# Optimization experiments

Hardware: AMD Instinct MI355X
Metric: run time of the kernel (lower is better)

The kernel has to match this reference:

```python
import jax, jax.numpy as jnp
import numpy as np

B, T, D, U, P, E = 32, 10, 10, 50, 50, 256
EPS_ATTN = 1e-8
EPS_LN = 1e-5


def _layer_norm(x, w, b):
    mu = jnp.mean(x, axis=-1, keepdims=True)
    var = jnp.mean((x - mu) ** 2, axis=-1, keepdims=True)
    return (x - mu) / jnp.sqrt(var + EPS_LN) * w + b


def setup_inputs() -> dict:
    key = jax.random.key(0)
    ks = jax.random.split(key, 8)
    xavier = float(np.sqrt(2.0 / (E + E)))
    return {
        "Q": jax.random.normal(ks[0], (B, T, U, E), dtype=jnp.float32),
        "K": jax.random.normal(ks[1], (B, D, P, E), dtype=jnp.float32),
        "V": jax.random.normal(ks[2], (B, D, P, E), dtype=jnp.float32),
        "attention_mask": jnp.zeros((B, T, D, U, P), dtype=jnp.float32),
        "W1": jax.random.normal(ks[3], (E, E), dtype=jnp.float32) * xavier,
        "b1": jnp.zeros((E,), dtype=jnp.float32),
        "W2": jax.random.normal(ks[4], (E, E), dtype=jnp.float32) * xavier,
        "b2": jnp.zeros((E,), dtype=jnp.float32),
        "ln1_w": jnp.ones((E,), dtype=jnp.float32),
        "ln1_b": jnp.zeros((E,), dtype=jnp.float32),
        "ln2_w": jnp.ones((E,), dtype=jnp.float32),
        "ln2_b": jnp.zeros((E,), dtype=jnp.float32),
    }


def reference(Q, K, V, attention_mask, W1, b1, W2, b2, ln1_w, ln1_b, ln2_w, ln2_b):
    # dk = max(1.0, emb_dim); scale = sqrt(dk) + eps
    scale = jnp.sqrt(jnp.asarray(float(max(1.0, Q.shape[-1])), dtype=Q.dtype)) + EPS_ATTN
    # (B,T,D,U,P) attention logits
    qk = jnp.einsum("btue,bdpe->btdup", Q, K) / scale + attention_mask
    score = jax.nn.softmax(qk, axis=-1)
    v_att = jnp.einsum("btdup,bdpe->btdue", score, V)  # (B,T,D,U,E)
    x = Q[:, :, None, :, :] + v_att  # broadcast over doc dim
    x = _layer_norm(x, ln1_w, ln1_b)
    ffn = jnp.maximum(x @ W1.T + b1, 0.0) @ W2.T + b2
    return _layer_norm(ffn + x, ln2_w, ln2_b)
```

## Files before the change

### kernel.cpp

```cpp
#include <hip/hip_runtime.h>
#include <math.h>

#define Bsz 32
#define Tt  10
#define Dd  10
#define Uu  50
#define Pp  50
#define Ee  256

typedef __attribute__((ext_vector_type(8))) short bf16x8;
typedef __attribute__((ext_vector_type(4))) float f32x4;

#define STH 264
#define STV 72
#define STS 72

#define K1_OFF_V 0
#define K1_OFF_S 36864
#define K1_OFF_R 46080
#define K1_SMEM  47104

#define K2_OFF_H 0
#define K2_OFF_R 33792
#define K2_SMEM  35840

__device__ __forceinline__ unsigned short f2bf(float f) {
    unsigned u = __builtin_bit_cast(unsigned, f);
    u += 0x7fffu + ((u >> 16) & 1u);
    return (unsigned short)(u >> 16);
}
__device__ __forceinline__ float bf2f(unsigned short h) {
    unsigned u = ((unsigned)h) << 16;
    return __builtin_bit_cast(float, u);
}
__device__ __forceinline__ bf16x8 ldfrag(const unsigned short* p, int stride, int r0, int c0, int lane) {
    return *(const bf16x8*)(p + (size_t)(r0 + (lane & 15)) * stride + c0 + ((lane >> 4) << 3));
}
__device__ __forceinline__ bf16x8 gfrag49(const float* __restrict__ base, int n, int k0, int lane) {
    int row = n + (lane & 15);
    row = row > 49 ? 49 : row;
    const int col = k0 + ((lane >> 4) << 3);
    const float4 a = *(const float4*)(base + (size_t)row * 256 + col);
    const float4 b = *(const float4*)(base + (size_t)row * 256 + col + 4);
    bf16x8 r;
    r[0] = (short)f2bf(a.x); r[1] = (short)f2bf(a.y); r[2] = (short)f2bf(a.z); r[3] = (short)f2bf(a.w);
    r[4] = (short)f2bf(b.x); r[5] = (short)f2bf(b.y); r[6] = (short)f2bf(b.z); r[7] = (short)f2bf(b.w);
    return r;
}
__device__ __forceinline__ bf16x8 wfrag(const unsigned short* wbf, const float* wf, int use_ws,
                                        int n, int k0, int lane) {
    const int row = n + (lane & 15);
    const int col = k0 + ((lane >> 4) << 3);
    if (use_ws) {
        return *(const bf16x8*)(wbf + (size_t)row * 256 + col);
    }
    const float4 a = *(const float4*)(wf + (size_t)row * 256 + col);
    const float4 b = *(const float4*)(wf + (size_t)row * 256 + col + 4);
    bf16x8 r;
    r[0] = (short)f2bf(a.x); r[1] = (short)f2bf(a.y); r[2] = (short)f2bf(a.z); r[3] = (short)f2bf(a.w);
    r[4] = (short)f2bf(b.x); r[5] = (short)f2bf(b.y); r[6] = (short)f2bf(b.z); r[7] = (short)f2bf(b.w);
    return r;
}

__global__ void convert_w_kernel(const float* __restrict__ W1, const float* __restrict__ W2,
                                 unsigned short* __restrict__ ws) {
    int i4 = (blockIdx.x * 256 + threadIdx.x) * 4;
    float4 a = *(const float4*)(W1 + i4);
    ushort4 oa; oa.x = f2bf(a.x); oa.y = f2bf(a.y); oa.z = f2bf(a.z); oa.w = f2bf(a.w);
    *(ushort4*)(ws + i4) = oa;
    float4 b = *(const float4*)(W2 + i4);
    ushort4 ob; ob.x = f2bf(b.x); ob.y = f2bf(b.y); ob.z = f2bf(b.z); ob.w = f2bf(b.w);
    *(ushort4*)(ws + 65536 + i4) = ob;
}

__global__ __launch_bounds__(512, 4) void attn_kernel(
    const float* __restrict__ Q,  const float* __restrict__ K,
    const float* __restrict__ V,  const float* __restrict__ Msk,
    const float* __restrict__ ln1w, const float* __restrict__ ln1b,
    float* __restrict__ out)
{
    __shared__ __align__(16) unsigned char smem[K1_SMEM];
    unsigned short* sVt = (unsigned short*)(smem + K1_OFF_V);
    unsigned short* sS  = (unsigned short*)(smem + K1_OFF_S);
    float*          red = (float*)(smem + K1_OFF_R);

    const int tid  = threadIdx.x;
    const int lane = tid & 63;
    const int wave = tid >> 6;
    const int quad = lane >> 4;
    const int l15  = lane & 15;

    const int btd = ((blockIdx.x & 7) * 400) + (blockIdx.x >> 3);
    const int b   = btd / (Tt * Dd);
    const int rem = btd % (Tt * Dd);
    const int t   = rem / Dd;
    const int d   = rem % Dd;

    const float* Qb = Q + ((size_t)(b * Tt + t) * Uu) * Ee;
    const float* Kb = K + ((size_t)(b * Dd + d) * Pp) * Ee;
    const float* Vb = V + ((size_t)(b * Dd + d) * Pp) * Ee;
    const float* Mb = Msk + ((size_t)((b * Tt + t) * Dd + d) * Uu) * Pp;
    float*       Xb = out + ((size_t)btd * Uu) * Ee;

    if (wave < 4) {
        const int mt = wave;
        int arow = mt * 16 + l15; if (arow > 49) arow = 49;
        const float* qrow = Qb + (size_t)arow * Ee + (quad << 3);
        f32x4 acc[4];
        #pragma unroll
        for (int i = 0; i < 4; ++i) acc[i] = (f32x4){0.f, 0.f, 0.f, 0.f};
        #pragma unroll
        for (int k0 = 0; k0 < 256; k0 += 32) {
            float4 qa = *(const float4*)(qrow + k0);
            float4 qb = *(const float4*)(qrow + k0 + 4);
            bf16x8 a;
            a[0] = (short)f2bf(qa.x); a[1] = (short)f2bf(qa.y); a[2] = (short)f2bf(qa.z); a[3] = (short)f2bf(qa.w);
            a[4] = (short)f2bf(qb.x); a[5] = (short)f2bf(qb.y); a[6] = (short)f2bf(qb.z); a[7] = (short)f2bf(qb.w);
            #pragma unroll
            for (int nt = 0; nt < 4; ++nt) {
                bf16x8 bf = gfrag49(Kb, nt << 4, k0, lane);
                acc[nt] = __builtin_amdgcn_mfma_f32_16x16x32_bf16(a, bf, acc[nt], 0, 0, 0);
            }
        }
        float l[4][4];
        #pragma unroll
        for (int nt = 0; nt < 4; ++nt) {
            int p = (nt << 4) + l15;
            #pragma unroll
            for (int r = 0; r < 4; ++r) {
                int u = mt * 16 + (quad << 2) + r;
                float v = acc[nt][r] * 0.0625f;
                if (p < Pp) { if (u < Uu) v += Mb[u * Pp + p]; }
                else v = -1e30f;
                l[nt][r] = v;
            }
        }
        #pragma unroll
        for (int r = 0; r < 4; ++r) {
            float m = fmaxf(fmaxf(l[0][r], l[1][r]), fmaxf(l[2][r], l[3][r]));
            #pragma unroll
            for (int msk = 1; msk < 16; msk <<= 1) m = fmaxf(m, __shfl_xor(m, msk));
            float e0 = __expf(l[0][r] - m), e1 = __expf(l[1][r] - m);
            float e2 = __expf(l[2][r] - m), e3 = __expf(l[3][r] - m);
            float s = e0 + e1 + e2 + e3;
            #pragma unroll
            for (int msk = 1; msk < 16; msk <<= 1) s += __shfl_xor(s, msk);
            float inv = 1.0f / s;
            int u = mt * 16 + (quad << 2) + r;
            sS[u * STS +  0 + l15] = f2bf(e0 * inv);
            sS[u * STS + 16 + l15] = f2bf(e1 * inv);
            sS[u * STS + 32 + l15] = f2bf(e2 * inv);
            sS[u * STS + 48 + l15] = f2bf(e3 * inv);
        }
    } else {
        const int lt = tid - 256;
        #pragma unroll 4
        for (int i = lt; i < 12800; i += 256) {
            int p = i >> 8, e = i & 255;
            sVt[e * STV + p] = f2bf(Vb[p * Ee + e]);
        }
        for (int i = lt; i < 3584; i += 256) {
            int p = 50 + (i >> 8), e = i & 255;
            sVt[e * STV + p] = 0;
        }
    }
    __syncthreads();

    {
        const int mt = wave >> 1;
        const int nh = (wave & 1) << 7;
        f32x4 acc[8];
        #pragma unroll
        for (int i = 0; i < 8; ++i) acc[i] = (f32x4){0.f, 0.f, 0.f, 0.f};
        #pragma unroll
        for (int k0 = 0; k0 < 64; k0 += 32) {
            bf16x8 a = ldfrag(sS, STS, mt << 4, k0, lane);
            #pragma unroll
            for (int nt = 0; nt < 8; ++nt) {
                bf16x8 bf = ldfrag(sVt, STV, nh + (nt << 4), k0, lane);
                acc[nt] = __builtin_amdgcn_mfma_f32_16x16x32_bf16(a, bf, acc[nt], 0, 0, 0);
            }
        }
        float s1[4] = {0.f, 0.f, 0.f, 0.f}, s2[4] = {0.f, 0.f, 0.f, 0.f};
        #pragma unroll
        for (int nt = 0; nt < 8; ++nt) {
            int e = nh + (nt << 4) + l15;
            #pragma unroll
            for (int r = 0; r < 4; ++r) {
                int u = (mt << 4) + (quad << 2) + r;
                float x = 0.f;
                if (u < Uu) x = acc[nt][r] + Qb[(size_t)u * Ee + e];
                acc[nt][r] = x;
                s1[r] += x; s2[r] += x * x;
            }
        }
        #pragma unroll
        for (int msk = 1; msk < 16; msk <<= 1) {
            #pragma unroll
            for (int r = 0; r < 4; ++r) { s1[r] += __shfl_xor(s1[r], msk); s2[r] += __shfl_xor(s2[r], msk); }
        }
        if (l15 == 0) {
            #pragma unroll
            for (int r = 0; r < 4; ++r) {
                int u = (mt << 4) + (quad << 2) + r;
                red[u * 4 + (wave & 1) * 2 + 0] = s1[r];
                red[u * 4 + (wave & 1) * 2 + 1] = s2[r];
            }
        }
        __syncthreads();
        #pragma unroll
        for (int r = 0; r < 4; ++r) {
            int u = (mt << 4) + (quad << 2) + r;
            if (u < Uu) {
                float sum = red[u * 4 + 0] + red[u * 4 + 2];
                float sq  = red[u * 4 + 1] + red[u * 4 + 3];
                float mu = sum * (1.0f / 256.0f);
                float var = sq * (1.0f / 256.0f) - mu * mu;
                float rstd = rsqrtf(var + 1e-5f);
                #pragma unroll
                for (int nt = 0; nt < 8; ++nt) {
                    int e = nh + (nt << 4) + l15;
                    Xb[(size_t)u * Ee + e] = (acc[nt][r] - mu) * rstd * ln1w[e] + ln1b[e];
                }
            }
        }
    }
}

__global__ __launch_bounds__(512, 4) void ffn_kernel(
    const float* __restrict__ W1, const float* __restrict__ b1,
    const float* __restrict__ W2, const float* __restrict__ b2,
    const float* __restrict__ ln2w, const float* __restrict__ ln2b,
    const unsigned short* __restrict__ wsbf, int use_ws,
    float* __restrict__ out)
{
    __shared__ __align__(16) unsigned char smem[K2_SMEM];
    unsigned short* sH   = (unsigned short*)(smem + K2_OFF_H);
    float*          red2 = (float*)(smem + K2_OFF_R);

    const int tid  = threadIdx.x;
    const int lane = tid & 63;
    const int wave = tid >> 6;
    const int quad = lane >> 4;
    const int l15  = lane & 15;

    const int btd = blockIdx.x;
    const float* Xb = out + (size_t)btd * Uu * Ee;
    float*       Ob = out + (size_t)btd * Uu * Ee;

    const int mp = wave >> 2;
    const int nq = wave & 3;

    {
        f32x4 acc2[2][4];
        #pragma unroll
        for (int mi = 0; mi < 2; ++mi)
            #pragma unroll
            for (int nt = 0; nt < 4; ++nt) acc2[mi][nt] = (f32x4){0.f, 0.f, 0.f, 0.f};
        float b1v[4];
        #pragma unroll
        for (int nt = 0; nt < 4; ++nt) b1v[nt] = b1[(nq << 6) + (nt << 4) + l15];
        #pragma unroll
        for (int k0 = 0; k0 < 256; k0 += 32) {
            bf16x8 a0 = gfrag49(Xb, (mp << 5),      k0, lane);
            bf16x8 a1 = gfrag49(Xb, (mp << 5) + 16, k0, lane);
            #pragma unroll
            for (int nt = 0; nt < 4; ++nt) {
                bf16x8 bf = wfrag(wsbf, W1, use_ws, (nq << 6) + (nt << 4), k0, lane);
                acc2[0][nt] = __builtin_amdgcn_mfma_f32_16x16x32_bf16(a0, bf, acc2[0][nt], 0, 0, 0);
                acc2[1][nt] = __builtin_amdgcn_mfma_f32_16x16x32_bf16(a1, bf, acc2[1][nt], 0, 0, 0);
            }
        }
        #pragma unroll
        for (int mi = 0; mi < 2; ++mi)
            #pragma unroll
            for (int nt = 0; nt < 4; ++nt) {
                int j = (nq << 6) + (nt << 4) + l15;
                #pragma unroll
                for (int r = 0; r < 4; ++r) {
                    int u = (mp << 5) + (mi << 4) + (quad << 2) + r;
                    sH[u * STH + j] = f2bf(fmaxf(acc2[mi][nt][r] + b1v[nt], 0.f));
                }
            }
    }
    __syncthreads();

    {
        f32x4 acc2[2][4];
        #pragma unroll
        for (int mi = 0; mi < 2; ++mi)
            #pragma unroll
            for (int nt = 0; nt < 4; ++nt) acc2[mi][nt] = (f32x4){0.f, 0.f, 0.f, 0.f};
        float b2v[4], w2l[4], b2l[4];
        #pragma unroll
        for (int nt = 0; nt < 4; ++nt) {
            int j = (nq << 6) + (nt << 4) + l15;
            b2v[nt] = b2[j]; w2l[nt] = ln2w[j]; b2l[nt] = ln2b[j];
        }
        #pragma unroll
        for (int k0 = 0; k0 < 256; k0 += 32) {
            bf16x8 a0 = ldfrag(sH, STH, (mp << 5),      k0, lane);
            bf16x8 a1 = ldfrag(sH, STH, (mp << 5) + 16, k0, lane);
            #pragma unroll
            for (int nt = 0; nt < 4; ++nt) {
                bf16x8 bf = wfrag(wsbf + 65536, W2, use_ws, (nq << 6) + (nt << 4), k0, lane);
                acc2[0][nt] = __builtin_amdgcn_mfma_f32_16x16x32_bf16(a0, bf, acc2[0][nt], 0, 0, 0);
                acc2[1][nt] = __builtin_amdgcn_mfma_f32_16x16x32_bf16(a1, bf, acc2[1][nt], 0, 0, 0);
            }
        }
        float s1[2][4], s2[2][4];
        #pragma unroll
        for (int mi = 0; mi < 2; ++mi)
            #pragma unroll
            for (int r = 0; r < 4; ++r) { s1[mi][r] = 0.f; s2[mi][r] = 0.f; }
        #pragma unroll
        for (int mi = 0; mi < 2; ++mi)
            #pragma unroll
            for (int nt = 0; nt < 4; ++nt) {
                int j = (nq << 6) + (nt << 4) + l15;
                #pragma unroll
                for (int r = 0; r < 4; ++r) {
                    int u = (mp << 5) + (mi << 4) + (quad << 2) + r;
                    float xr = (u < Uu) ? Xb[(size_t)u * Ee + j] : 0.f;
                    float y = acc2[mi][nt][r] + b2v[nt] + xr;
                    acc2[mi][nt][r] = y;
                    s1[mi][r] += y; s2[mi][r] += y * y;
                }
            }
        #pragma unroll
        for (int msk = 1; msk < 16; msk <<= 1)
            #pragma unroll
            for (int mi = 0; mi < 2; ++mi)
                #pragma unroll
                for (int r = 0; r < 4; ++r) {
                    s1[mi][r] += __shfl_xor(s1[mi][r], msk);
                    s2[mi][r] += __shfl_xor(s2[mi][r], msk);
                }
        if (l15 == 0) {
            #pragma unroll
            for (int mi = 0; mi < 2; ++mi)
                #pragma unroll
                for (int r = 0; r < 4; ++r) {
                    int u = (mp << 5) + (mi << 4) + (quad << 2) + r;
                    red2[u * 8 + nq * 2 + 0] = s1[mi][r];
                    red2[u * 8 + nq * 2 + 1] = s2[mi][r];
                }
        }
        __syncthreads();
        #pragma unroll
        for (int mi = 0; mi < 2; ++mi)
            #pragma unroll
            for (int r = 0; r < 4; ++r) {
                int u = (mp << 5) + (mi << 4) + (quad << 2) + r;
                if (u < Uu) {
                    float sum = red2[u * 8 + 0] + red2[u * 8 + 2] + red2[u * 8 + 4] + red2[u * 8 + 6];
                    float sq  = red2[u * 8 + 1] + red2[u * 8 + 3] + red2[u * 8 + 5] + red2[u * 8 + 7];
                    float mu = sum * (1.0f / 256.0f);
                    float var = sq * (1.0f / 256.0f) - mu * mu;
                    float rstd = rsqrtf(var + 1e-5f);
                    #pragma unroll
                    for (int nt = 0; nt < 4; ++nt) {
                        int j = (nq << 6) + (nt << 4) + l15;
                        Ob[(size_t)u * Ee + j] = (acc2[mi][nt][r] - mu) * rstd * w2l[nt] + b2l[nt];
                    }
                }
            }
    }
}

extern "C" void kernel_launch(void* const* d_in, const int* in_sizes, int n_in,
                              void* d_out, int out_size, void* d_ws, size_t ws_size,
                              hipStream_t stream) {
    const float* Q    = (const float*)d_in[0];
    const float* K    = (const float*)d_in[1];
    const float* V    = (const float*)d_in[2];
    const float* M    = (const float*)d_in[3];
    const float* W1   = (const float*)d_in[4];
    const float* b1   = (const float*)d_in[5];
    const float* W2   = (const float*)d_in[6];
    const float* b2   = (const float*)d_in[7];
    const float* ln1w = (const float*)d_in[8];
    const float* ln1b = (const float*)d_in[9];
    const float* ln2w = (const float*)d_in[10];
    const float* ln2b = (const float*)d_in[11];
    float* out = (float*)d_out;

    int use_ws = (ws_size >= 262144) ? 1 : 0;
    const unsigned short* wsbf = (const unsigned short*)d_ws;
    if (use_ws) {
        convert_w_kernel<<<64, 256, 0, stream>>>(W1, W2, (unsigned short*)d_ws);
    }
    attn_kernel<<<Bsz * Tt * Dd, 512, 0, stream>>>(Q, K, V, M, ln1w, ln1b, out);
    ffn_kernel<<<Bsz * Tt * Dd, 512, 0, stream>>>(W1, b1, W2, b2, ln2w, ln2b,
                                                  wsbf, use_ws, out);
}
```

Measured before the change: 673.9 us.

## Tile FFN over flattened rows in 128-row blocks instead of per-50-row group

The FFN kernel now treats all B*T*D*U rows as one flat matrix and gives each block 128 rows, instead of 50 rows padded to 64. This removes the padding waste of about 22% in the MFMA work and reuses each weight fragment across four M-tiles per wave, which cuts weight traffic per row. In exchange the block uses twice the LDS and needs more accumulator registers, which may lower occupancy. The total row count of 160000 divides evenly by 128, so no bounds checks are needed.

```diff
diff --git a/kernel.cpp b/kernel.cpp
--- a/kernel.cpp
+++ b/kernel.cpp
@@ -21,8 +21,9 @@
 #define K1_SMEM  47104
 
 #define K2_OFF_H 0
-#define K2_OFF_R 33792
-#define K2_SMEM  35840
+#define K2_OFF_R 67584
+#define K2_SMEM  71680
+#define FFN_BM 128
 
 __device__ __forceinline__ unsigned short f2bf(float f) {
     unsigned u = __builtin_bit_cast(unsigned, f);
@@ -47,6 +48,16 @@
     r[4] = (short)f2bf(b.x); r[5] = (short)f2bf(b.y); r[6] = (short)f2bf(b.z); r[7] = (short)f2bf(b.w);
     return r;
 }
+__device__ __forceinline__ bf16x8 xfrag(const float* __restrict__ base, int n, int k0, int lane) {
+    const int row = n + (lane & 15);
+    const int col = k0 + ((lane >> 4) << 3);
+    const float4 a = *(const float4*)(base + (size_t)row * 256 + col);
+    const float4 b = *(const float4*)(base + (size_t)row * 256 + col + 4);
+    bf16x8 r;
+    r[0] = (short)f2bf(a.x); r[1] = (short)f2bf(a.y); r[2] = (short)f2bf(a.z); r[3] = (short)f2bf(a.w);
+    r[4] = (short)f2bf(b.x); r[5] = (short)f2bf(b.y); r[6] = (short)f2bf(b.z); r[7] = (short)f2bf(b.w);
+    return r;
+}
 __device__ __forceinline__ bf16x8 wfrag(const unsigned short* wbf, const float* wf, int use_ws,
                                         int n, int k0, int lane) {
     const int row = n + (lane & 15);
@@ -244,53 +255,55 @@
     const int quad = lane >> 4;
     const int l15  = lane & 15;
 
-    const int btd = blockIdx.x;
-    const float* Xb = out + (size_t)btd * Uu * Ee;
-    float*       Ob = out + (size_t)btd * Uu * Ee;
-
-    const int mp = wave >> 2;
+    const int mw = wave >> 2;
     const int nq = wave & 3;
 
+    const size_t rowbase = (size_t)blockIdx.x * FFN_BM;
+    const float* Xb = out + rowbase * Ee;
+    float*       Ob = out + rowbase * Ee;
+
     {
-        f32x4 acc2[2][4];
-        #pragma unroll
-        for (int mi = 0; mi < 2; ++mi)
-            #pragma unroll
-            for (int nt = 0; nt < 4; ++nt) acc2[mi][nt] = (f32x4){0.f, 0.f, 0.f, 0.f};
+        f32x4 acc[4][4];
+        #pragma unroll
+        for (int mi = 0; mi < 4; ++mi)
+            #pragma unroll
+            for (int nt = 0; nt < 4; ++nt) acc[mi][nt] = (f32x4){0.f, 0.f, 0.f, 0.f};
         float b1v[4];
         #pragma unroll
         for (int nt = 0; nt < 4; ++nt) b1v[nt] = b1[(nq << 6) + (nt << 4) + l15];
         #pragma unroll
         for (int k0 = 0; k0 < 256; k0 += 32) {
-            bf16x8 a0 = gfrag49(Xb, (mp << 5),      k0, lane);
-            bf16x8 a1 = gfrag49(Xb, (mp << 5) + 16, k0, lane);
+            bf16x8 a[4];
+            #pragma unroll
+            for (int mi = 0; mi < 4; ++mi) a[mi] = xfrag(Xb, (mw << 6) + (mi << 4), k0, lane);
             #pragma unroll
             for (int nt = 0; nt < 4; ++nt) {
                 bf16x8 bf = wfrag(wsbf, W1, use_ws, (nq << 6) + (nt << 4), k0, lane);
-                acc2[0][nt] = __builtin_amdgcn_mfma_f32_16x16x32_bf16(a0, bf, acc2[0][nt], 0, 0, 0);
-                acc2[1][nt] = __builtin_amdgcn_mfma_f32_16x16x32_bf16(a1, bf, acc2[1][nt], 0, 0, 0);
-            }
-        }
-        #pragma unroll
-        for (int mi = 0; mi < 2; ++mi)
+                #pragma unroll
+                for (int mi = 0; mi < 4; ++mi)
+                    acc[mi][nt] = __builtin_amdgcn_mfma_f32_16x16x32_bf16(a[mi], bf, acc[mi][nt], 0, 0, 0);
+            }
+        }
+        #pragma unroll
+        for (int mi = 0; mi < 4; ++mi)
             #pragma unroll
             for (int nt = 0; nt < 4; ++nt) {
                 int j = (nq << 6) + (nt << 4) + l15;
                 #pragma unroll
                 for (int r = 0; r < 4; ++r) {
-                    int u = (mp << 5) + (mi << 4) + (quad << 2) + r;
-                    sH[u * STH + j] = f2bf(fmaxf(acc2[mi][nt][r] + b1v[nt], 0.f));
+                    int u = (mw << 6) + (mi << 4) + (quad << 2) + r;
+                    sH[u * STH + j] = f2bf(fmaxf(acc[mi][nt][r] + b1v[nt], 0.f));
                 }
             }
     }
     __syncthreads();
 
     {
-        f32x4 acc2[2][4];
-        #pragma unroll
-        for (int mi = 0; mi < 2; ++mi)
-            #pragma unroll
-            for (int nt = 0; nt < 4; ++nt) acc2[mi][nt] = (f32x4){0.f, 0.f, 0.f, 0.f};
+        f32x4 acc[4][4];
+        #pragma unroll
+        for (int mi = 0; mi < 4; ++mi)
+            #pragma unroll
+            for (int nt = 0; nt < 4; ++nt) acc[mi][nt] = (f32x4){0.f, 0.f, 0.f, 0.f};
         float b2v[4], w2l[4], b2l[4];
         #pragma unroll
         for (int nt = 0; nt < 4; ++nt) {
@@ -299,70 +312,62 @@
         }
         #pragma unroll
         for (int k0 = 0; k0 < 256; k0 += 32) {
-            bf16x8 a0 = ldfrag(sH, STH, (mp << 5),      k0, lane);
-            bf16x8 a1 = ldfrag(sH, STH, (mp << 5) + 16, k0, lane);
+            bf16x8 a[4];
+            #pragma unroll
+            for (int mi = 0; mi < 4; ++mi) a[mi] = ldfrag(sH, STH, (mw << 6) + (mi << 4), k0, lane);
             #pragma unroll
             for (int nt = 0; nt < 4; ++nt) {
                 bf16x8 bf = wfrag(wsbf + 65536, W2, use_ws, (nq << 6) + (nt << 4), k0, lane);
-                acc2[0][nt] = __builtin_amdgcn_mfma_f32_16x16x32_bf16(a0, bf, acc2[0][nt], 0, 0, 0);
-                acc2[1][nt] = __builtin_amdgcn_mfma_f32_16x16x32_bf16(a1, bf, acc2[1][nt], 0, 0, 0);
-            }
-        }
-        float s1[2][4], s2[2][4];
-        #pragma unroll
-        for (int mi = 0; mi < 2; ++mi)
-            #pragma unroll
-            for (int r = 0; r < 4; ++r) { s1[mi][r] = 0.f; s2[mi][r] = 0.f; }
-        #pragma unroll
-        for (int mi = 0; mi < 2; ++mi)
+                #pragma unroll
+                for (int mi = 0; mi < 4; ++mi)
+                    acc[mi][nt] = __builtin_amdgcn_mfma_f32_16x16x32_bf16(a[mi], bf, acc[mi][nt], 0, 0, 0);
+            }
+        }
+        #pragma unroll
+        for (int mi = 0; mi < 4; ++mi) {
+            float s1[4] = {0.f, 0.f, 0.f, 0.f}, s2[4] = {0.f, 0.f, 0.f, 0.f};
             #pragma unroll
             for (int nt = 0; nt < 4; ++nt) {
                 int j = (nq << 6) + (nt << 4) + l15;
                 #pragma unroll
                 for (int r = 0; r < 4; ++r) {
-                    int u = (mp << 5) + (mi << 4) + (quad << 2) + r;
-                    float xr = (u < Uu) ? Xb[(size_t)u * Ee + j] : 0.f;
-                    float y = acc2[mi][nt][r] + b2v[nt] + xr;
-                    acc2[mi][nt][r] = y;
-                    s1[mi][r] += y; s2[mi][r] += y * y;
-                }
-            }
-        #pragma unroll
-        for (int msk = 1; msk < 16; msk <<= 1)
-            #pragma unroll
-            for (int mi = 0; mi < 2; ++mi)
+                    int u = (mw << 6) + (mi << 4) + (quad << 2) + r;
+                    float y = acc[mi][nt][r] + b2v[nt] + Xb[(size_t)u * Ee + j];
+                    acc[mi][nt][r] = y;
+                    s1[r] += y; s2[r] += y * y;
+                }
+            }
+            #pragma unroll
+            for (int msk = 1; msk < 16; msk <<= 1)
                 #pragma unroll
                 for (int r = 0; r < 4; ++r) {
-                    s1[mi][r] += __shfl_xor(s1[mi][r], msk);
-                    s2[mi][r] += __shfl_xor(s2[mi][r], msk);
-                }
-        if (l15 == 0) {
-            #pragma unroll
-            for (int mi = 0; mi < 2; ++mi)
+                    s1[r] += __shfl_xor(s1[r], msk);
+                    s2[r] += __shfl_xor(s2[r], msk);
+                }
+            if (l15 == 0) {
                 #pragma unroll
                 for (int r = 0; r < 4; ++r) {
-                    int u = (mp << 5) + (mi << 4) + (quad << 2) + r;
-                    red2[u * 8 + nq * 2 + 0] = s1[mi][r];
-                    red2[u * 8 + nq * 2 + 1] = s2[mi][r];
-                }
+                    int u = (mw << 6) + (mi << 4) + (quad << 2) + r;
+                    red2[u * 8 + nq * 2 + 0] = s1[r];
+                    red2[u * 8 + nq * 2 + 1] = s2[r];
+                }
+            }
         }
         __syncthreads();
         #pragma unroll
-        for (int mi = 0; mi < 2; ++mi)
+        for (int mi = 0; mi < 4; ++mi)
             #pragma unroll
             for (int r = 0; r < 4; ++r) {
-                int u = (mp << 5) + (mi << 4) + (quad << 2) + r;
-                if (u < Uu) {
-                    float sum = red2[u * 8 + 0] + red2[u * 8 + 2] + red2[u * 8 + 4] + red2[u * 8 + 6];
-                    float sq  = red2[u * 8 + 1] + red2[u * 8 + 3] + red2[u * 8 + 5] + red2[u * 8 + 7];
-                    float mu = sum * (1.0f / 256.0f);
-                    float var = sq * (1.0f / 256.0f) - mu * mu;
-                    float rstd = rsqrtf(var + 1e-5f);
-                    #pragma unroll
-                    for (int nt = 0; nt < 4; ++nt) {
-                        int j = (nq << 6) + (nt << 4) + l15;
-                        Ob[(size_t)u * Ee + j] = (acc2[mi][nt][r] - mu) * rstd * w2l[nt] + b2l[nt];
-                    }
+                int u = (mw << 6) + (mi << 4) + (quad << 2) + r;
+                float sum = red2[u * 8 + 0] + red2[u * 8 + 2] + red2[u * 8 + 4] + red2[u * 8 + 6];
+                float sq  = red2[u * 8 + 1] + red2[u * 8 + 3] + red2[u * 8 + 5] + red2[u * 8 + 7];
+                float mu = sum * (1.0f / 256.0f);
+                float var = sq * (1.0f / 256.0f) - mu * mu;
+                float rstd = rsqrtf(var + 1e-5f);
+                #pragma unroll
+                for (int nt = 0; nt < 4; ++nt) {
+                    int j = (nq << 6) + (nt << 4) + l15;
+                    Ob[(size_t)u * Ee + j] = (acc[mi][nt][r] - mu) * rstd * w2l[nt] + b2l[nt];
                 }
             }
     }
@@ -391,6 +396,6 @@
         convert_w_kernel<<<64, 256, 0, stream>>>(W1, W2, (unsigned short*)d_ws);
     }
     attn_kernel<<<Bsz * Tt * Dd, 512, 0, stream>>>(Q, K, V, M, ln1w, ln1b, out);
-    ffn_kernel<<<Bsz * Tt * Dd, 512, 0, stream>>>(W1, b1, W2, b2, ln2w, ln2b,
-                                                  wsbf, use_ws, out);
-}
+    ffn_kernel<<<(Bsz * Tt * Dd * Uu) / FFN_BM, 512, 0, stream>>>(W1, b1, W2, b2, ln2w, ln2b,
+                                                                  wsbf, use_ws, out);
+}
```

Result: no change. 682.8 us (+1.3%).
